# Optimization experiments

Hardware: AMD Instinct MI355X
Metric: run time of the kernel (lower is better)

The kernel has to match this reference:

```python
import jax, jax.numpy as jnp
import numpy as np

B, S, D, H = 4, 2048, 1024, 16
DK = D // H

def setup_inputs() -> dict:
    key = jax.random.key(0)
    k1, k2, k3 = jax.random.split(key, 3)
    x = jax.random.normal(k1, (B, S, D), dtype=jnp.float32)
    # kaiming-uniform-ish scale for (d_k, d_model) fan_in = d_model
    bound = 1.0 / np.sqrt(D)
    w_qkv = jax.random.uniform(k2, (3, H, DK, D), dtype=jnp.float32, minval=-bound, maxval=bound)
    w_o = jax.random.uniform(k3, (D, D), dtype=jnp.float32, minval=-bound, maxval=bound)
    return {"x": x, "w_qkv": w_qkv, "w_o": w_o}

def reference(x, w_qkv, w_o):
    seq_len = x.shape[-2]
    d_k = w_qkv.shape[-2]
    # qkv projection: (b s m),(qkv h k m) -> (qkv b h s k)
    qkv = jnp.einsum('bsm,qhkm->qbhsk', x, w_qkv)
    Q, K, V = qkv[0], qkv[1], qkv[2]
    scores = jnp.einsum('bhqk,bhsk->bhqs', Q, K) / jnp.sqrt(jnp.float32(d_k))
    causal = jnp.triu(jnp.ones((seq_len, seq_len), dtype=bool), k=1)
    scores = jnp.where(causal, -jnp.inf, scores)
    probs = jax.nn.softmax(scores, axis=-1)  # (b h s s)
    attn = jnp.einsum('bhqs,bhsk->bhqk', probs, V)
    # concat heads: (b h s k) -> (b s h*k)
    attn = jnp.transpose(attn, (0, 2, 1, 3)).reshape(x.shape[0], seq_len, -1)
    # out proj: y = attn @ w_o.T
    return jnp.einsum('bsd,md->bsm', attn, w_o)
```

## Files before the change

### kernel.cpp

```cpp
#include <hip/hip_runtime.h>
#include <stdint.h>
#include <stddef.h>

typedef unsigned short u16;
typedef float  f32x4  __attribute__((ext_vector_type(4)));
typedef short  s16x8  __attribute__((ext_vector_type(8)));
typedef short  s16x4  __attribute__((ext_vector_type(4)));
typedef __bf16 bf16x8 __attribute__((ext_vector_type(8)));
typedef __bf16 bf16x4 __attribute__((ext_vector_type(4)));
typedef u16    u16x4  __attribute__((ext_vector_type(4)));

#define DEV static __device__ __forceinline__

DEV u16 f2bf(float f){
  uint32_t u = __builtin_bit_cast(uint32_t, f);
  u += 0x7FFFu + ((u >> 16) & 1u);
  return (u16)(u >> 16);
}

DEV f32x4 mfma16(s16x8 a, s16x8 b, f32x4 c){
  return __builtin_amdgcn_mfma_f32_16x16x32_bf16(
      __builtin_bit_cast(bf16x8, a), __builtin_bit_cast(bf16x8, b), c, 0, 0, 0);
}

DEV f32x4 mfma16k(s16x4 a, s16x4 b, f32x4 c){
  return __builtin_amdgcn_mfma_f32_16x16x16bf16_1k(a, b, c, 0, 0, 0);
}

DEV float exp2_fast(float x){ return __builtin_exp2f(x); }

DEV void gl_lds16(const u16* g, u16* l){
  __builtin_amdgcn_global_load_lds(
      (__attribute__((address_space(1))) void*)(g),
      (__attribute__((address_space(3))) void*)(l), 16, 0, 0);
}

__global__ __launch_bounds__(256) void cvt_all(const float* __restrict__ x,
                                               const float* __restrict__ wqkv,
                                               const float* __restrict__ wo,
                                               u16* __restrict__ outb){
  const int N1 = 2097152;
  const int N2 = N1 + 786432;
  const int NT = N2 + 262144;
  const int stride = gridDim.x * blockDim.x;
  for (int i = blockIdx.x * blockDim.x + threadIdx.x; i < NT; i += stride){
    const float* src; int j;
    if (i < N1){ src = x; j = i; }
    else if (i < N2){ src = wqkv; j = i - N1; }
    else { src = wo; j = i - N2; }
    float4 v = *(const float4*)(src + (size_t)j * 4);
    u16x4 o = { f2bf(v.x), f2bf(v.y), f2bf(v.z), f2bf(v.w) };
    *(u16x4*)(outb + (size_t)i * 4) = o;
  }
}

template<bool SWAPOP>
DEV void gemm_core(const u16* __restrict__ A, const u16* __restrict__ Bw,
                   int K, int bm, int bn, u16* ldsA, u16* ldsB, f32x4 acc[4][4])
{
  const int lane = threadIdx.x & 63;
  const int wave = threadIdx.x >> 6;
  const int wm = (wave >> 1) * 64, wn = (wave & 1) * 64;
  const int l8 = (lane & 7) * 8;
  const int lr = lane >> 3;
  const int fr = lane & 15;
  const int k8 = (lane >> 4) * 8;

  #pragma unroll
  for (int m = 0; m < 4; m++)
    #pragma unroll
    for (int n = 0; n < 4; n++){ f32x4 z = {0.f,0.f,0.f,0.f}; acc[m][n] = z; }

  const int nkt = K >> 6;
  for (int kt = 0; kt < nkt; ++kt){
    const int kb = kt * 64;
    #pragma unroll
    for (int i = 0; i < 4; i++){
      const int c   = wave * 4 + i;
      const int row = c * 8 + lr;
      gl_lds16(A  + (size_t)(bm + row) * K + kb + l8, ldsA + c * 512);
      gl_lds16(Bw + (size_t)(bn + row) * K + kb + l8, ldsB + c * 512);
    }
    __syncthreads();
    #pragma unroll
    for (int kk = 0; kk < 2; ++kk){
      s16x8 af[4], bfr[4];
      #pragma unroll
      for (int m = 0; m < 4; m++) af[m]  = *(const s16x8*)(ldsA + (wm + m*16 + fr)*64 + kk*32 + k8);
      #pragma unroll
      for (int n = 0; n < 4; n++) bfr[n] = *(const s16x8*)(ldsB + (wn + n*16 + fr)*64 + kk*32 + k8);
      #pragma unroll
      for (int m = 0; m < 4; m++)
        #pragma unroll
        for (int n = 0; n < 4; n++)
          acc[m][n] = SWAPOP ? mfma16(bfr[n], af[m], acc[m][n])
                             : mfma16(af[m], bfr[n], acc[m][n]);
    }
    __syncthreads();
  }
}

__global__ __launch_bounds__(256) void gemm_qkv(const u16* __restrict__ xb,
                                                const u16* __restrict__ wb,
                                                u16* __restrict__ Qd,
                                                u16* __restrict__ Kd,
                                                u16* __restrict__ Vtd)
{
  __shared__ __align__(16) u16 ldsA[128*64];
  __shared__ __align__(16) u16 ldsB[128*64];
  f32x4 acc[4][4];
  const int bm = blockIdx.x * 128, bn = blockIdx.y * 128;
  const int q = bn >> 10;

  const int lane = threadIdx.x & 63, wave = threadIdx.x >> 6;
  const int wm = (wave >> 1) * 64, wn = (wave & 1) * 64;
  const int fr = lane & 15, r4 = (lane >> 4) * 4;

  if (q < 2){
    gemm_core<true>(xb, wb, 1024, bm, bn, ldsA, ldsB, acc);
    #pragma unroll
    for (int m = 0; m < 4; m++){
      const int s  = bm + wm + m*16 + fr;
      const int b  = s >> 11;
      const int s0 = s & 2047;
      #pragma unroll
      for (int n = 0; n < 4; n++){
        const int ng0 = bn + wn + n*16 + r4;
        const int h   = (ng0 >> 6) & 15, kd0 = ng0 & 63;
        const size_t bh = (size_t)(b * 16 + h);
        if (q == 0){
          u16x4 v = { f2bf(acc[m][n][0] * 0.18033688011112042f),
                      f2bf(acc[m][n][1] * 0.18033688011112042f),
                      f2bf(acc[m][n][2] * 0.18033688011112042f),
                      f2bf(acc[m][n][3] * 0.18033688011112042f) };
          *(u16x4*)(Qd + (bh*2048 + s0)*64 + kd0) = v;
        } else {
          u16x4 v = { f2bf(acc[m][n][0]), f2bf(acc[m][n][1]),
                      f2bf(acc[m][n][2]), f2bf(acc[m][n][3]) };
          *(u16x4*)(Kd + (bh*2048 + s0)*64 + kd0) = v;
        }
      }
    }
  } else {
    gemm_core<false>(xb, wb, 1024, bm, bn, ldsA, ldsB, acc);
    #pragma unroll
    for (int m = 0; m < 4; m++){
      const int i0 = bm + wm + m*16 + r4;
      const int b  = i0 >> 11;
      const int s0 = i0 & 2047;
      #pragma unroll
      for (int n = 0; n < 4; n++){
        const int ng = bn + wn + n*16 + fr;
        const int h  = (ng >> 6) & 15, kd = ng & 63;
        const size_t bh = (size_t)(b * 16 + h);
        u16x4 v = { f2bf(acc[m][n][0]), f2bf(acc[m][n][1]),
                    f2bf(acc[m][n][2]), f2bf(acc[m][n][3]) };
        *(u16x4*)(Vtd + (bh*64 + kd)*2048 + s0) = v;
      }
    }
  }
}

__global__ __launch_bounds__(256) void gemm_outp(const u16* __restrict__ attnb,
                                                 const u16* __restrict__ wob,
                                                 float* __restrict__ C)
{
  __shared__ __align__(16) u16 ldsA[128*64];
  __shared__ __align__(16) u16 ldsB[128*64];
  f32x4 acc[4][4];
  const int bm = blockIdx.x * 128, bn = blockIdx.y * 128;
  gemm_core<true>(attnb, wob, 1024, bm, bn, ldsA, ldsB, acc);

  const int lane = threadIdx.x & 63, wave = threadIdx.x >> 6;
  const int wm = (wave >> 1) * 64, wn = (wave & 1) * 64;
  const int fr = lane & 15, r4 = (lane >> 4) * 4;
  #pragma unroll
  for (int m = 0; m < 4; m++){
    const int i0 = bm + wm + m*16 + fr;
    #pragma unroll
    for (int n = 0; n < 4; n++){
      const int ng0 = bn + wn + n*16 + r4;
      *(f32x4*)(C + (size_t)i0 * 1024 + ng0) = acc[m][n];
    }
  }
}

DEV void chunk_step1(const u16* Kc, const u16* Vc, int kb, int q0,
                     const s16x8 (&qf)[2], f32x4 (&O)[4], f32x4 &L,
                     float &mrun, s16x4 ones,
                     int fr, int g, int f, int r4)
{
  f32x4 sc[4];
  #pragma unroll
  for (int mi = 0; mi < 4; mi++){ f32x4 z = {0.f,0.f,0.f,0.f}; sc[mi] = z; }
  __builtin_amdgcn_s_setprio(1);
  #pragma unroll
  for (int kk = 0; kk < 2; kk++)
    #pragma unroll
    for (int mi = 0; mi < 4; mi++){
      s16x8 kf = *(const s16x8*)(Kc + (mi*16 + fr)*64 + ((kk*4 + g) ^ f)*8);
      sc[mi] = mfma16(kf, qf[kk], sc[mi]);
    }
  __builtin_amdgcn_s_setprio(0);

  const int q_g = q0 + fr;
  float tmax = -1e30f;
  if (kb + 63 > q0){
    #pragma unroll
    for (int mi = 0; mi < 4; mi++)
      #pragma unroll
      for (int r = 0; r < 4; r++){
        const int s_g = kb + mi*16 + r4 + r;
        float v = sc[mi][r];
        v = (s_g > q_g) ? -1e30f : v;
        sc[mi][r] = v;
        tmax = fmaxf(tmax, v);
      }
  } else {
    #pragma unroll
    for (int mi = 0; mi < 4; mi++)
      #pragma unroll
      for (int r = 0; r < 4; r++)
        tmax = fmaxf(tmax, sc[mi][r]);
  }
  float m_new = mrun;
  if (!__all(tmax <= m_new + 8.f)){
    float tm = fmaxf(tmax, __shfl_xor(tmax, 16));
    tm = fmaxf(tm, __shfl_xor(tm, 32));
    m_new = fmaxf(m_new, tm);
    const float corr = exp2_fast(mrun - m_new);
    mrun = m_new;
    L[0] *= corr;
    #pragma unroll
    for (int n = 0; n < 4; n++)
      #pragma unroll
      for (int r = 0; r < 4; r++)
        O[n][r] *= corr;
  }
  s16x4 pb[4];
  #pragma unroll
  for (int mi = 0; mi < 4; mi++){
    f32x4 e;
    #pragma unroll
    for (int r = 0; r < 4; r++)
      e[r] = exp2_fast(sc[mi][r] - m_new);
    pb[mi] = __builtin_bit_cast(s16x4, __builtin_convertvector(e, bf16x4));
  }

  __builtin_amdgcn_s_setprio(1);
  #pragma unroll
  for (int mi = 0; mi < 4; mi++){
    L = mfma16k(ones, pb[mi], L);
    #pragma unroll
    for (int n = 0; n < 4; n++){
      s16x4 vf = *(const s16x4*)(Vc + (n*16 + fr)*64 + ((2*mi + (g >> 1)) ^ f)*8 + (g & 1)*4);
      O[n] = mfma16k(vf, pb[mi], O[n]);
    }
  }
  __builtin_amdgcn_s_setprio(0);
}

__global__ __launch_bounds__(256, 4) void attn_fwd(const u16* __restrict__ Qd,
                                                   const u16* __restrict__ Kd,
                                                   const u16* __restrict__ Vtd,
                                                   u16* __restrict__ attnb)
{
  __shared__ __align__(16) u16 Kl[2][64*64];
  __shared__ __align__(16) u16 Vl[2][64*64];

  const int t = threadIdx.x;
  const int lane = t & 63, w = t >> 6;
  const int wg = blockIdx.x;
  const int bh = 8 * (wg & 7) + (wg >> 7);
  const int ph = (wg >> 3) & 15;
  const int p  = ph >> 1, half = ph & 1;
  const int qh = 8 + p, ql = 7 - p;
  const u16* Qp = Qd  + (size_t)bh * 2048 * 64;
  const u16* Kp = Kd  + (size_t)bh * 2048 * 64;
  const u16* Vp = Vtd + (size_t)bh * 64 * 2048;

  const int fr = lane & 15, g = lane >> 4;
  const int f  = fr & 7;
  const int k8 = g * 8, r4 = g * 4;
  const int rgs = half * 4 + w;
  const int qh0 = qh * 128 + rgs * 16;
  const int ql0 = ql * 128 + rgs * 16;
  const int nkt = 2 * qh + 2;

  const s16x4 ones = { 0x3F80, 0x3F80, 0x3F80, 0x3F80 };

  s16x8 qfh[2], qfl[2];
  #pragma unroll
  for (int kk = 0; kk < 2; kk++){
    qfh[kk] = *(const s16x8*)(Qp + (size_t)(qh0 + fr) * 64 + kk*32 + k8);
    qfl[kk] = *(const s16x8*)(Qp + (size_t)(ql0 + fr) * 64 + kk*32 + k8);
  }

  f32x4 Ohi[4], Olo[4], Lhi, Llo;
  #pragma unroll
  for (int n = 0; n < 4; n++){
    f32x4 z = {0.f,0.f,0.f,0.f}; Ohi[n] = z; Olo[n] = z;
  }
  { f32x4 z = {0.f,0.f,0.f,0.f}; Lhi = z; Llo = z; }
  float mh = -1e30f, ml = -1e30f;

  const int Lr  = t >> 3;
  const int cs8 = ((t & 7) ^ (Lr & 7)) * 8;
  const u16* kS = Kp + Lr * 64 + cs8;
  const u16* vS = Vp + (size_t)Lr * 2048 + cs8;

  gl_lds16(kS,         (u16*)Kl + t*8);
  gl_lds16(kS + 2048,  (u16*)Kl + t*8 + 2048);
  gl_lds16(vS,         (u16*)Vl + t*8);
  gl_lds16(vS + 65536, (u16*)Vl + t*8 + 2048);
  kS += 4096; vS += 64;

  for (int kt = 0; kt < nkt; ++kt){
    __syncthreads();
    const int cur = kt & 1;
    if (kt + 1 < nkt){
      u16* kD = (u16*)Kl + (cur ^ 1) * 4096 + t*8;
      u16* vD = (u16*)Vl + (cur ^ 1) * 4096 + t*8;
      gl_lds16(kS,         kD);
      gl_lds16(kS + 2048,  kD + 2048);
      gl_lds16(vS,         vD);
      gl_lds16(vS + 65536, vD + 2048);
    }
    kS += 4096; vS += 64;

    const int kb = kt * 64;
    const u16* Kc = Kl[cur];
    const u16* Vc = Vl[cur];

    if (kb <= qh0 + 15)
      chunk_step1(Kc, Vc, kb, qh0, qfh, Ohi, Lhi, mh, ones, fr, g, f, r4);
    if (kb <= ql0 + 15)
      chunk_step1(Kc, Vc, kb, ql0, qfl, Olo, Llo, ml, ones, fr, g, f, r4);
  }

  const int b = bh >> 4, h = bh & 15;
  const float invh = 1.0f / Lhi[0];
  const float invl = 1.0f / Llo[0];
  const int sh = qh0 + fr;
  const int sl = ql0 + fr;
  #pragma unroll
  for (int n = 0; n < 4; n++){
    u16x4 vh = { f2bf(Ohi[n][0]*invh), f2bf(Ohi[n][1]*invh),
                 f2bf(Ohi[n][2]*invh), f2bf(Ohi[n][3]*invh) };
    *(u16x4*)(attnb + (((size_t)b*2048 + sh)*16 + h)*64 + n*16 + r4) = vh;
    u16x4 vl = { f2bf(Olo[n][0]*invl), f2bf(Olo[n][1]*invl),
                 f2bf(Olo[n][2]*invl), f2bf(Olo[n][3]*invl) };
    *(u16x4*)(attnb + (((size_t)b*2048 + sl)*16 + h)*64 + n*16 + r4) = vl;
  }
}

extern "C" void kernel_launch(void* const* d_in, const int* in_sizes, int n_in,
                              void* d_out, int out_size, void* d_ws, size_t ws_size,
                              hipStream_t stream)
{
  const float* x    = (const float*)d_in[0];
  const float* wqkv = (const float*)d_in[1];
  const float* wo   = (const float*)d_in[2];
  float* out = (float*)d_out;

  char* ws = (char*)d_ws;
  u16* xb    = (u16*)(ws);
  u16* wqb   = (u16*)(ws + 16777216);
  u16* wob   = (u16*)(ws + 23068672);
  u16* Qd    = (u16*)(ws + 25165824);
  u16* Kd    = (u16*)(ws + 41943040);
  u16* Vtd   = (u16*)(ws + 58720256);
  u16* attnb = xb;

  cvt_all<<<3072, 256, 0, stream>>>(x, wqkv, wo, xb);
  gemm_qkv<<<dim3(64, 24), 256, 0, stream>>>(xb, wqb, Qd, Kd, Vtd);
  attn_fwd<<<dim3(1024), 256, 0, stream>>>(Qd, Kd, Vtd, attnb);
  gemm_outp<<<dim3(64, 8), 256, 0, stream>>>(attnb, wob, out);
}
```

Baseline: 204.7 us.

## Double-buffer LDS tiles in GEMM core with async prefetch two stages ahead

Reworks the shared GEMM mainloop used by the QKV and output projections. It now double-buffers the A/B tiles in LDS, prefetching tile kt+2 through global_load_lds while the current tile is computed. Explicit vmcnt waits and raw s_barrier with sched barriers replace __syncthreads, and wave priority is raised around the MFMA section. The goal is to hide global memory latency behind compute. The cost is twice the LDS per block, which may lower occupancy, and hand-tuned waitcnt counts that must match the number of outstanding loads.

```diff
diff --git a/kernel.cpp b/kernel.cpp
--- a/kernel.cpp
+++ b/kernel.cpp
@@ -34,6 +34,9 @@
       (__attribute__((address_space(1))) void*)(g),
       (__attribute__((address_space(3))) void*)(l), 16, 0, 0);
 }
+
+DEV void fence_sched(){ __builtin_amdgcn_sched_barrier(0); }
+DEV void bar_raw(){ fence_sched(); __builtin_amdgcn_s_barrier(); fence_sched(); }
 
 __global__ __launch_bounds__(256) void cvt_all(const float* __restrict__ x,
                                                const float* __restrict__ wqkv,
@@ -61,34 +64,47 @@
   const int lane = threadIdx.x & 63;
   const int wave = threadIdx.x >> 6;
   const int wm = (wave >> 1) * 64, wn = (wave & 1) * 64;
-  const int l8 = (lane & 7) * 8;
-  const int lr = lane >> 3;
   const int fr = lane & 15;
   const int k8 = (lane >> 4) * 8;
+  const int c0 = wave * 4;
 
   #pragma unroll
   for (int m = 0; m < 4; m++)
     #pragma unroll
     for (int n = 0; n < 4; n++){ f32x4 z = {0.f,0.f,0.f,0.f}; acc[m][n] = z; }
+
+  const u16* aS = A  + (size_t)(bm + c0*8 + (lane >> 3)) * K + (lane & 7) * 8;
+  const u16* bS = Bw + (size_t)(bn + c0*8 + (lane >> 3)) * K + (lane & 7) * 8;
+
+  #pragma unroll
+  for (int i = 0; i < 4; i++){
+    gl_lds16(aS + (size_t)i*8*K, ldsA + (c0 + i) * 512);
+    gl_lds16(bS + (size_t)i*8*K, ldsB + (c0 + i) * 512);
+  }
+  #pragma unroll
+  for (int i = 0; i < 4; i++){
+    gl_lds16(aS + (size_t)i*8*K + 64, ldsA + 8192 + (c0 + i) * 512);
+    gl_lds16(bS + (size_t)i*8*K + 64, ldsB + 8192 + (c0 + i) * 512);
+  }
 
   const int nkt = K >> 6;
   for (int kt = 0; kt < nkt; ++kt){
-    const int kb = kt * 64;
-    #pragma unroll
-    for (int i = 0; i < 4; i++){
-      const int c   = wave * 4 + i;
-      const int row = c * 8 + lr;
-      gl_lds16(A  + (size_t)(bm + row) * K + kb + l8, ldsA + c * 512);
-      gl_lds16(Bw + (size_t)(bn + row) * K + kb + l8, ldsB + c * 512);
-    }
-    __syncthreads();
+    const int cur = (kt & 1) * 8192;
+    fence_sched();
+    if (kt + 1 < nkt) asm volatile("s_waitcnt vmcnt(8)" ::: "memory");
+    else              asm volatile("s_waitcnt vmcnt(0)" ::: "memory");
+    bar_raw();
+
+    const u16* As = ldsA + cur;
+    const u16* Bs = ldsB + cur;
+    __builtin_amdgcn_s_setprio(1);
     #pragma unroll
     for (int kk = 0; kk < 2; ++kk){
       s16x8 af[4], bfr[4];
       #pragma unroll
-      for (int m = 0; m < 4; m++) af[m]  = *(const s16x8*)(ldsA + (wm + m*16 + fr)*64 + kk*32 + k8);
-      #pragma unroll
-      for (int n = 0; n < 4; n++) bfr[n] = *(const s16x8*)(ldsB + (wn + n*16 + fr)*64 + kk*32 + k8);
+      for (int m = 0; m < 4; m++) af[m]  = *(const s16x8*)(As + (wm + m*16 + fr)*64 + kk*32 + k8);
+      #pragma unroll
+      for (int n = 0; n < 4; n++) bfr[n] = *(const s16x8*)(Bs + (wn + n*16 + fr)*64 + kk*32 + k8);
       #pragma unroll
       for (int m = 0; m < 4; m++)
         #pragma unroll
@@ -96,7 +112,19 @@
           acc[m][n] = SWAPOP ? mfma16(bfr[n], af[m], acc[m][n])
                              : mfma16(af[m], bfr[n], acc[m][n]);
     }
-    __syncthreads();
+    __builtin_amdgcn_s_setprio(0);
+
+    bar_raw();
+    if (kt + 2 < nkt){
+      const size_t kb2 = (size_t)(kt + 2) << 6;
+      u16* dA = ldsA + cur;
+      u16* dB = ldsB + cur;
+      #pragma unroll
+      for (int i = 0; i < 4; i++){
+        gl_lds16(aS + (size_t)i*8*K + kb2, dA + (c0 + i) * 512);
+        gl_lds16(bS + (size_t)i*8*K + kb2, dB + (c0 + i) * 512);
+      }
+    }
   }
 }
 
@@ -106,8 +134,8 @@
                                                 u16* __restrict__ Kd,
                                                 u16* __restrict__ Vtd)
 {
-  __shared__ __align__(16) u16 ldsA[128*64];
-  __shared__ __align__(16) u16 ldsB[128*64];
+  __shared__ __align__(16) u16 ldsA[2*128*64];
+  __shared__ __align__(16) u16 ldsB[2*128*64];
   f32x4 acc[4][4];
   const int bm = blockIdx.x * 128, bn = blockIdx.y * 128;
   const int q = bn >> 10;
@@ -165,8 +193,8 @@
                                                  const u16* __restrict__ wob,
                                                  float* __restrict__ C)
 {
-  __shared__ __align__(16) u16 ldsA[128*64];
-  __shared__ __align__(16) u16 ldsB[128*64];
+  __shared__ __align__(16) u16 ldsA[2*128*64];
+  __shared__ __align__(16) u16 ldsB[2*128*64];
   f32x4 acc[4][4];
   const int bm = blockIdx.x * 128, bn = blockIdx.y * 128;
   gemm_core<true>(attnb, wob, 1024, bm, bn, ldsA, ldsB, acc);
```

New measurement: 203.1 us. About the same (-0.8%).
